# Optimization experiments

Hardware: AMD Instinct MI355X
Metric: run time of the kernel (lower is better)

## Reference

```python
import jax, jax.numpy as jnp
import numpy as np

N_NODES = 100000
N_EDGES = 1600000
NEG_SLOPE = 0.2
EPS = 1e-6


def setup_inputs() -> dict:
    key = jax.random.key(0)
    ks = jax.random.split(key, 14)
    s = 0.1  # weight init scale
    return {
        "x": jax.random.normal(ks[0], (N_NODES, 64), jnp.float32),
        "src": jax.random.randint(ks[1], (N_EDGES,), 0, N_NODES, jnp.int32),
        "dst": jax.random.randint(ks[2], (N_EDGES,), 0, N_NODES, jnp.int32),
        "W0": s * jax.random.normal(ks[3], (64, 128), jnp.float32),
        "al0": s * jax.random.normal(ks[4], (4, 32), jnp.float32),
        "ar0": s * jax.random.normal(ks[5], (4, 32), jnp.float32),
        "W1": s * jax.random.normal(ks[6], (128, 128), jnp.float32),
        "al1": s * jax.random.normal(ks[7], (4, 32), jnp.float32),
        "ar1": s * jax.random.normal(ks[8], (4, 32), jnp.float32),
        "resW1": s * jax.random.normal(ks[9], (128, 128), jnp.float32),
        "W2": s * jax.random.normal(ks[10], (128, 32), jnp.float32),
        "al2": s * jax.random.normal(ks[11], (1, 32), jnp.float32),
        "ar2": s * jax.random.normal(ks[12], (1, 32), jnp.float32),
        "resW2": s * jax.random.normal(ks[13], (128, 32), jnp.float32),
    }


def gat_conv(h, src, dst, W, al, ar, resW):
    """DGL-style GATConv. h: [N, Fin]; returns [N, H, D]."""
    H, D = al.shape
    feat = (h @ W).reshape(-1, H, D)                       # [N,H,D]
    el = jnp.sum(feat * al, axis=-1)                       # [N,H]
    er = jnp.sum(feat * ar, axis=-1)                       # [N,H]
    e = jax.nn.leaky_relu(el[src] + er[dst], NEG_SLOPE)    # [E,H]
    # segment softmax over destination nodes
    m = jax.ops.segment_max(e, dst, num_segments=N_NODES)  # [N,H]
    ex = jnp.exp(e - m[dst])                               # [E,H]
    denom = jax.ops.segment_sum(ex, dst, num_segments=N_NODES)
    alpha = ex / denom[dst]                                # [E,H]
    msg = alpha[:, :, None] * feat[src]                    # [E,H,D]
    rst = jax.ops.segment_sum(msg, dst, num_segments=N_NODES)  # [N,H,D]
    if resW is not None:
        rst = rst + (h @ resW).reshape(-1, H, D)
    return rst


def pairnorm_scs(x, scale=1.0):
    # 'PN-SCS' mode: scale-individually then center by original column mean
    col_mean = jnp.mean(x, axis=0)
    rownorm = jnp.sqrt(EPS + jnp.sum(x * x, axis=1, keepdims=True))
    return scale * x / rownorm - col_mean


def reference(x, src, dst, W0, al0, ar0, W1, al1, ar1, resW1, W2, al2, ar2, resW2):
    # layer 0: no residual, activation applied outside
    h = gat_conv(x, src, dst, W0, al0, ar0, None)          # [N,4,32]
    h = jax.nn.elu(h.reshape(h.shape[0], -1))              # [N,128]
    h = pairnorm_scs(h)
    # middle layer: residual + internal ELU (DGL applies activation inside),
    # then the outer loop flattens and applies ELU again
    h = jax.nn.elu(gat_conv(h, src, dst, W1, al1, ar1, resW1))  # [N,4,32]
    h = jax.nn.elu(h.reshape(h.shape[0], -1))              # [N,128]
    h = pairnorm_scs(h)
    # final layer: residual, mean over heads
    h = gat_conv(h, src, dst, W2, al2, ar2, resW2)         # [N,1,32]
    h = jnp.mean(h, axis=1)                                # [N,32]
    # dgl.mean_nodes readout on a single graph -> mean over nodes
    return jnp.mean(h, axis=0)                             # [32]
```

## Files before the change

kernel.cpp:

```cpp
#include <hip/hip_runtime.h>


typedef __attribute__((ext_vector_type(8))) short s8v;
typedef __attribute__((ext_vector_type(4))) float f4v;
typedef __attribute__((ext_vector_type(2))) float f2v;
typedef __attribute__((ext_vector_type(2))) _Float16 h2;
typedef __attribute__((ext_vector_type(4))) _Float16 h4;

__device__ __forceinline__ unsigned short f2bf(float f) {
  unsigned int x = __float_as_uint(f);
  x += 0x7fffu + ((x >> 16) & 1u);
  return (unsigned short)(x >> 16);
}
__device__ __forceinline__ float bf2f(unsigned short u) {
  return __uint_as_float(((unsigned int)u) << 16);
}
__device__ __forceinline__ unsigned short f2h(float f) {
  _Float16 h = (_Float16)f;
  return __builtin_bit_cast(unsigned short, h);
}
__device__ __forceinline__ unsigned char f2fp8(float v) {
  return (unsigned char)(__builtin_amdgcn_cvt_pk_fp8_f32(v, v, 0, false) & 0xff);
}
__device__ __forceinline__ float lrelu(float x) { return fmaxf(x, 0.2f * x); }
__device__ __forceinline__ float elu1(float x) { return x > 0.f ? x : expm1f(x); }

__global__ __launch_bounds__(256) void hist2_k(const int* __restrict__ dst, int* __restrict__ counts,
                                               int* __restrict__ bhist, int E, int NB, int chunk) {
  __shared__ int h[512];
  for (int b = threadIdx.x; b < NB; b += 256) h[b] = 0;
  __syncthreads();
  int e0 = blockIdx.x * chunk;
  int e1 = min(E, e0 + chunk);
  for (int e = e0 + threadIdx.x; e < e1; e += 256) {
    int d = dst[e];
    atomicAdd(&counts[d], 1);
    atomicAdd(&h[d >> 8], 1);
  }
  __syncthreads();
  for (int b = threadIdx.x; b < NB; b += 256)
    bhist[(size_t)b * gridDim.x + blockIdx.x] = h[b];
}

__global__ __launch_bounds__(256) void scanA(const int* __restrict__ counts, int* __restrict__ rsp,
                                             int* __restrict__ bsumA, int* __restrict__ bhist,
                                             int* __restrict__ bsumB, int NA, int NSEG, int nbA) {
  __shared__ int s[256];
  int t = threadIdx.x;
  bool isA = (int)blockIdx.x < nbA;
  int bb = isA ? (int)blockIdx.x : (int)blockIdx.x - nbA;
  const int* in = isA ? counts : bhist;
  int* out = isA ? rsp : bhist;
  int* bs = isA ? bsumA : bsumB;
  int Nn = isA ? NA : NSEG;
  int base = bb * 1024 + t * 4;
  int v0 = (base + 0 < Nn) ? in[base + 0] : 0;
  int v1 = (base + 1 < Nn) ? in[base + 1] : 0;
  int v2 = (base + 2 < Nn) ? in[base + 2] : 0;
  int v3 = (base + 3 < Nn) ? in[base + 3] : 0;
  if (isA) {
    v0 = (v0 + 15) & ~15;
    v1 = (v1 + 15) & ~15;
    v2 = (v2 + 15) & ~15;
    v3 = (v3 + 15) & ~15;
  }
  s[t] = v0 + v1 + v2 + v3;
  __syncthreads();
  for (int off = 1; off < 256; off <<= 1) {
    int xv = (t >= off) ? s[t - off] : 0;
    __syncthreads();
    s[t] += xv;
    __syncthreads();
  }
  int excl = t ? s[t - 1] : 0;
  if (t == 255) bs[bb] = s[255];
  if (base + 0 < Nn) { out[base + 0] = excl; excl += v0; }
  if (base + 1 < Nn) { out[base + 1] = excl; excl += v1; }
  if (base + 2 < Nn) { out[base + 2] = excl; excl += v2; }
  if (base + 3 < Nn) { out[base + 3] = excl; }
}

__global__ __launch_bounds__(256) void scanB(int* __restrict__ rsp, const int* __restrict__ bsumA,
                                             int* __restrict__ bhist, const int* __restrict__ bsumB,
                                             int NA, int NSEG, int nbA, int nbB) {
  __shared__ int s[256];
  int t = threadIdx.x;
  bool isA = (int)blockIdx.x < nbA;
  int bb = isA ? (int)blockIdx.x : (int)blockIdx.x - nbA;
  int* arr = isA ? rsp : bhist;
  const int* bs = isA ? bsumA : bsumB;
  int nb = isA ? nbA : nbB;
  int Nn = isA ? NA : NSEG;
  s[t] = (t < nb) ? bs[t] : 0;
  __syncthreads();
  for (int off = 1; off < 256; off <<= 1) {
    int xv = (t >= off) ? s[t - off] : 0;
    __syncthreads();
    s[t] += xv;
    __syncthreads();
  }
  int pref = bb ? s[bb - 1] : 0;
  if (pref != 0) {
    int base = bb * 1024 + t * 4;
    if (base + 0 < Nn) arr[base + 0] += pref;
    if (base + 1 < Nn) arr[base + 1] += pref;
    if (base + 2 < Nn) arr[base + 2] += pref;
    if (base + 3 < Nn) arr[base + 3] += pref;
  }
}

__global__ __launch_bounds__(256) void bscatter_k(const int* __restrict__ src, const int* __restrict__ dst,
                                                  const int* __restrict__ seg, int2* __restrict__ ebuf,
                                                  int E, int NB, int chunk) {
  __shared__ int cur[512];
  for (int b = threadIdx.x; b < NB; b += 256)
    cur[b] = seg[(size_t)b * gridDim.x + blockIdx.x];
  __syncthreads();
  int e0 = blockIdx.x * chunk;
  int e1 = min(E, e0 + chunk);
  for (int e = e0 + threadIdx.x; e < e1; e += 256) {
    int d = dst[e];
    int pos = atomicAdd(&cur[d >> 8], 1);
    int2 v; v.x = src[e]; v.y = d;
    ebuf[pos] = v;
  }
}

__global__ __launch_bounds__(256) void fscatter_k(const int2* __restrict__ ebuf, const int* __restrict__ seg,
                                                  const int* __restrict__ rsp, int* __restrict__ csr_src,
                                                  int E, int NB, int P2B, int Nn) {
  __shared__ int cur[256];
  int b = blockIdx.x;
  int node0 = b << 8;
  int node = node0 + threadIdx.x;
  if (node < Nn) cur[threadIdx.x] = rsp[node];
  __syncthreads();
  int bstart = seg[(size_t)b * P2B];
  int bend = (b + 1 < NB) ? seg[(size_t)(b + 1) * P2B] : E;
  for (int e = bstart + threadIdx.x; e < bend; e += 256) {
    int2 sd = ebuf[e];
    int pos = atomicAdd(&cur[sd.y - node0], 1);
    csr_src[pos] = sd.x;
  }
}

__device__ __forceinline__ void pack_one(const float* W, const float* al, const float* ar,
                                         const float* resW, unsigned short* out,
                                         int K, int M, int BF, int H, int RES0, int t) {
  int c = t / K, k = t - c * K;
  float v = 0.f;
  if (c < BF) {
    v = W[k * BF + c];
  } else if (c < BF + H) {
    int h = c - BF;
    float s = 0.f;
    for (int d = 0; d < 32; d++) s += W[k * BF + h * 32 + d] * al[h * 32 + d];
    v = s;
  } else if (c < BF + 2 * H) {
    int h = c - BF - H;
    float s = 0.f;
    for (int d = 0; d < 32; d++) s += W[k * BF + h * 32 + d] * ar[h * 32 + d];
    v = s;
  } else if (c >= RES0) {
    v = resW[k * (M - RES0) + (c - RES0)];
  }
  unsigned short hi = f2bf(v);
  out[c * K + k] = hi;
  out[M * K + c * K + k] = f2bf(v - bf2f(hi));
}

__global__ __launch_bounds__(256) void fill_all(const float* __restrict__ W0, const float* __restrict__ al0,
                                                const float* __restrict__ ar0,
                                                const float* __restrict__ W1, const float* __restrict__ al1,
                                                const float* __restrict__ ar1, const float* __restrict__ resW1,
                                                const float* __restrict__ W2, const float* __restrict__ al2,
                                                const float* __restrict__ ar2, const float* __restrict__ resW2,
                                                unsigned short* __restrict__ w0t, unsigned short* __restrict__ w1t,
                                                unsigned short* __restrict__ w2t) {
  const int n0 = 144 * 64, n1 = 272 * 128, n2 = 80 * 128;
  int t = blockIdx.x * 256 + threadIdx.x;
  if (t < n0) {
    pack_one(W0, al0, ar0, nullptr, w0t, 64, 144, 128, 4, 144, t);
  } else if (t < n0 + n1) {
    pack_one(W1, al1, ar1, resW1, w1t, 128, 272, 128, 4, 144, t - n0);
  } else if (t < n0 + n1 + n2) {
    pack_one(W2, al2, ar2, resW2, w2t, 128, 80, 32, 1, 48, t - n0 - n1);
  }
}

template <int K, int M, int R, int BF, int H, int RES0, bool AF32, bool CMW>
__global__ __launch_bounds__(256) void gemm_bf16(const void* __restrict__ Av,
                                                 const unsigned short* __restrict__ Bt,
                                                 const float* __restrict__ colsum, float invN,
                                                 unsigned char* __restrict__ feat8,
                                                 float* __restrict__ el, float* __restrict__ er,
                                                 unsigned short* __restrict__ resh, int nRowTiles) {
  __shared__ float cmw_s[M];
  if constexpr (CMW) {
    for (int cc = threadIdx.x; cc < M; cc += 256) {
      float s = 0.f;
      for (int k = 0; k < K; k++)
        s += colsum[k] * (bf2f(Bt[cc * K + k]) + bf2f(Bt[(size_t)M * K + cc * K + k]));
      cmw_s[cc] = s * invN;
    }
    __syncthreads();
  }
  int wv = (int)((blockIdx.x * blockDim.x + threadIdx.x) >> 6);
  int tile0 = wv * R;
  if (tile0 >= nRowTiles) return;
  int lane = threadIdx.x & 63;
  int r = lane & 15, q = lane >> 4;
  s8v afrag[R][K / 32];
#pragma unroll
  for (int rr = 0; rr < R; rr++) {
    if constexpr (AF32) {
      const float* arow = (const float*)Av + (size_t)((tile0 + rr) * 16 + r) * K + q * 8;
#pragma unroll
      for (int kk = 0; kk < K / 32; kk++) {
        s8v v;
#pragma unroll
        for (int j = 0; j < 8; j++) v[j] = (short)f2bf(arow[kk * 32 + j]);
        afrag[rr][kk] = v;
      }
    } else {
      const unsigned short* arow = (const unsigned short*)Av + (size_t)((tile0 + rr) * 16 + r) * K + q * 8;
#pragma unroll
      for (int kk = 0; kk < K / 32; kk++) afrag[rr][kk] = *(const s8v*)(arow + kk * 32);
    }
  }
#pragma unroll
  for (int ct = 0; ct < M / 16; ct++) {
    const unsigned short* brow = Bt + (size_t)(ct * 16 + r) * K + q * 8;
    s8v bhi[K / 32], blo[K / 32];
#pragma unroll
    for (int kk = 0; kk < K / 32; kk++) {
      bhi[kk] = *(const s8v*)(brow + kk * 32);
      blo[kk] = *(const s8v*)(brow + (size_t)M * K + kk * 32);
    }
    int col = ct * 16 + r;
    float cmwv = 0.f;
    if constexpr (CMW) cmwv = cmw_s[col];
#pragma unroll
    for (int rr = 0; rr < R; rr++) {
      f4v acc = {0.f, 0.f, 0.f, 0.f};
#pragma unroll
      for (int kk = 0; kk < K / 32; kk++) {
        acc = __builtin_amdgcn_mfma_f32_16x16x32_bf16(afrag[rr][kk], bhi[kk], acc, 0, 0, 0);
        acc = __builtin_amdgcn_mfma_f32_16x16x32_bf16(afrag[rr][kk], blo[kk], acc, 0, 0, 0);
      }
      int row0 = (tile0 + rr) * 16 + q * 4;
#pragma unroll
      for (int i = 0; i < 4; i++) {
        float v = acc[i] - cmwv;
        size_t row = (size_t)(row0 + i);
        if (col < BF) {
          feat8[row * BF + col] = f2fp8(v);
        } else if (col < BF + H) {
          el[row * H + (col - BF)] = v;
        } else if (col < BF + 2 * H) {
          er[row * H + (col - BF - H)] = v;
        } else if (RES0 < M && col >= RES0) {
          resh[row * (M - RES0) + (col - RES0)] = f2h(v);
        }
      }
    }
  }
}

template <int MODE>
__global__ __launch_bounds__(256) void aggregate4(const unsigned char* __restrict__ feat8,
                                                  const float* __restrict__ el4,
                                                  const float* __restrict__ er4,
                                                  const int* __restrict__ csr_src,
                                                  const int* __restrict__ rsp,
                                                  const int* __restrict__ counts,
                                                  const unsigned short* __restrict__ resh,
                                                  unsigned short* __restrict__ vbf,
                                                  float* __restrict__ rnrm, int Nn) {
  int n = (int)((blockIdx.x * blockDim.x + threadIdx.x) >> 6);
  if (n >= Nn) return;
  int lane = threadIdx.x & 63;
  int start = __builtin_amdgcn_readfirstlane(rsp[n]);
  int deg = __builtin_amdgcn_readfirstlane(counts[n]);
  int chunks = (deg + 15) >> 4;
  int slot = lane >> 2, h = lane & 3;
  float ern = er4[(size_t)n * 4 + h];
  int hl = lane >> 4;
  unsigned dby = (unsigned)lane << 1;
  f2v a01 = {0.f, 0.f};
  float dsum = 0.f;
  for (int c = 0; c < chunks; c++) {
    const int* csp = csr_src + start + (c << 4);
    int sA = csp[slot];
    float exv = 0.f;
    if (((c << 4) + slot) < deg) {
      float e = el4[(size_t)sA * 4 + h] + ern;
      exv = __expf(fmaxf(e, 0.2f * e));
    }
    dsum += exv;
    int sj[16];
#pragma unroll
    for (int j = 0; j < 16; j++) sj[j] = csp[j];
#pragma unroll
    for (int j = 0; j < 16; j++) {
      float aw = __shfl(exv, (j << 2) | hl);
      unsigned short u = *(const unsigned short*)(feat8 + (((unsigned)sj[j] << 7) + dby));
      f2v fv = __builtin_amdgcn_cvt_pk_f32_fp8((int)u, false);
      f2v aw2 = {aw, aw};
      a01 = __builtin_elementwise_fma(fv, aw2, a01);
    }
  }
#pragma unroll
  for (int off = 4; off < 64; off <<= 1) dsum += __shfl_xor(dsum, off);
  float inv = dsum > 0.f ? 1.f / dsum : 0.f;
  float invh = __shfl(inv, hl);
  float v0, v1;
  if (MODE == 1) {
    h2 rr = *(const h2*)(resh + (size_t)n * 128 + lane * 2);
    v0 = elu1(elu1(a01[0] * invh + (float)rr[0]));
    v1 = elu1(elu1(a01[1] * invh + (float)rr[1]));
  } else {
    v0 = elu1(a01[0] * invh);
    v1 = elu1(a01[1] * invh);
  }
  float ss = v0 * v0 + v1 * v1;
#pragma unroll
  for (int off = 1; off < 64; off <<= 1) ss += __shfl_xor(ss, off);
  float rn = sqrtf(1e-6f + ss);
  float ri = 1.f / rn;
  unsigned int pk = (unsigned int)f2bf(v0 * ri) | ((unsigned int)f2bf(v1 * ri) << 16);
  *(unsigned int*)((char*)vbf + ((size_t)n << 8) + (lane << 2)) = pk;
  if (lane == 0) rnrm[n] = rn;
}

__global__ __launch_bounds__(256) void aggregate1(const unsigned char* __restrict__ feat8,
                                                  const float* __restrict__ el1,
                                                  const float* __restrict__ er1,
                                                  const int* __restrict__ csr_src,
                                                  const int* __restrict__ rsp,
                                                  const int* __restrict__ counts,
                                                  const unsigned short* __restrict__ res2h,
                                                  float* __restrict__ out2, int Nn) {
  int n = (int)((blockIdx.x * blockDim.x + threadIdx.x) >> 6);
  if (n >= Nn) return;
  int lane = threadIdx.x & 63;
  int start = __builtin_amdgcn_readfirstlane(rsp[n]);
  int deg = __builtin_amdgcn_readfirstlane(counts[n]);
  int chunks = (deg + 15) >> 4;
  int l16 = lane & 15;
  float ern = er1[n];
  int g = lane >> 3;
  unsigned dofs4 = (unsigned)(lane & 7) << 2;
  f2v acc01 = {0.f, 0.f}, acc23 = {0.f, 0.f};
  float dsum = 0.f;
  for (int c = 0; c < chunks; c++) {
    const int* csp = csr_src + start + (c << 4);
    int sA = csp[l16];
    float exv = 0.f;
    if (((c << 4) + l16) < deg) exv = __expf(lrelu(el1[sA] + ern));
    dsum += exv;
#pragma unroll
    for (int t = 0; t < 2; t++) {
      int j = (t << 3) + g;
      int sj = __shfl(sA, j);
      float aw = __shfl(exv, j);
      f2v aw2 = {aw, aw};
      unsigned int u = *(const unsigned int*)(feat8 + (((unsigned)sj << 5) + dofs4));
      f2v fa = __builtin_amdgcn_cvt_pk_f32_fp8((int)u, false);
      f2v fb = __builtin_amdgcn_cvt_pk_f32_fp8((int)u, true);
      acc01 = __builtin_elementwise_fma(fa, aw2, acc01);
      acc23 = __builtin_elementwise_fma(fb, aw2, acc23);
    }
  }
#pragma unroll
  for (int off = 1; off < 16; off <<= 1) dsum += __shfl_xor(dsum, off);
  float inv = dsum > 0.f ? 1.f / dsum : 0.f;
#pragma unroll
  for (int off = 8; off < 64; off <<= 1) {
    acc01[0] += __shfl_xor(acc01[0], off);
    acc01[1] += __shfl_xor(acc01[1], off);
    acc23[0] += __shfl_xor(acc23[0], off);
    acc23[1] += __shfl_xor(acc23[1], off);
  }
  if (lane < 8) {
    h4 rr = *(const h4*)(res2h + (size_t)n * 32 + (lane << 2));
    float4 o;
    o.x = acc01[0] * inv + (float)rr[0];
    o.y = acc01[1] * inv + (float)rr[1];
    o.z = acc23[0] * inv + (float)rr[2];
    o.w = acc23[1] * inv + (float)rr[3];
    *(float4*)(out2 + (size_t)n * 32 + (lane << 2)) = o;
  }
}

__global__ __launch_bounds__(256) void colsum_k(const unsigned short* __restrict__ vbf,
                                                const float* __restrict__ rnrm,
                                                float* __restrict__ colsum, int Nn) {
  __shared__ float ls[256];
  int tid = threadIdx.x;
  int c = tid & 127, rsub = tid >> 7;
  float cs = 0.f;
  for (int r = blockIdx.x * 2 + rsub; r < Nn; r += gridDim.x * 2)
    cs += bf2f(vbf[(size_t)r * 128 + c]) * rnrm[r];
  ls[tid] = cs;
  __syncthreads();
  if (tid < 128) atomicAdd(&colsum[tid], ls[tid] + ls[tid + 128]);
}

__global__ __launch_bounds__(256) void final_reduce(const float* __restrict__ out2,
                                                    float* __restrict__ outsum, int Nn) {
  __shared__ float ls[32];
  if (threadIdx.x < 32) ls[threadIdx.x] = 0.f;
  __syncthreads();
  int d = threadIdx.x & 31, rl = threadIdx.x >> 5;
  float acc = 0.f;
  for (int n = blockIdx.x * 8 + rl; n < Nn; n += gridDim.x * 8)
    acc += out2[(size_t)n * 32 + d];
  atomicAdd(&ls[d], acc);
  __syncthreads();
  if (threadIdx.x < 32) atomicAdd(&outsum[threadIdx.x], ls[threadIdx.x]);
}

__global__ void finalize_k(const float* __restrict__ outsum, float* __restrict__ out, float invN) {
  int t = threadIdx.x;
  if (t < 32) out[t] = outsum[t] * invN;
}

extern "C" void kernel_launch(void* const* d_in, const int* in_sizes, int n_in,
                              void* d_out, int out_size, void* d_ws, size_t ws_size,
                              hipStream_t stream) {
  const float* x     = (const float*)d_in[0];
  const int*   src   = (const int*)d_in[1];
  const int*   dst   = (const int*)d_in[2];
  const float* W0    = (const float*)d_in[3];
  const float* al0   = (const float*)d_in[4];
  const float* ar0   = (const float*)d_in[5];
  const float* W1    = (const float*)d_in[6];
  const float* al1   = (const float*)d_in[7];
  const float* ar1   = (const float*)d_in[8];
  const float* resW1 = (const float*)d_in[9];
  const float* W2    = (const float*)d_in[10];
  const float* al2   = (const float*)d_in[11];
  const float* ar2   = (const float*)d_in[12];
  const float* resW2 = (const float*)d_in[13];
  const int N = in_sizes[0] / 64;
  const int E = in_sizes[1];
  const float invN = 1.f / (float)N;
  const int Emax = E + 15 * N + 1024;
  const int NB = (N + 255) >> 8;
  const int P2B = 512;
  const int chunk = (E + P2B - 1) / P2B;
  const int segN = NB * P2B;
  const int nbA = (N + 1023) / 1024;
  const int nbB = (segN + 1023) / 1024;

  char* p = (char*)d_ws;
  auto alloc = [&](size_t bytes) { char* r = p; p += (bytes + 255) & ~(size_t)255; return r; };

  char* zbase = p;
  int*   counts  = (int*)alloc((size_t)4 * N);
  float* colsumA = (float*)alloc(512);
  float* colsumB = (float*)alloc(512);
  float* outsum  = (float*)alloc(128);
  size_t zbytes = (size_t)(p - zbase);

  int* rsp   = (int*)alloc((size_t)4 * N);
  int* bsumA = (int*)alloc(1024);
  int* bhist = (int*)alloc((size_t)4 * segN);
  int* bsumB = (int*)alloc(1024);
  int2* ebuf = (int2*)alloc((size_t)8 * E);
  int* csr_src = (int*)alloc((size_t)4 * Emax);
  unsigned char*  feat8 = (unsigned char*)alloc((size_t)N * 128);
  unsigned short* vbf   = (unsigned short*)alloc((size_t)2 * N * 128);
  unsigned short* resh  = (unsigned short*)alloc((size_t)2 * N * 128);
  unsigned short* w0t = (unsigned short*)alloc((size_t)2 * 2 * 144 * 64);
  unsigned short* w1t = (unsigned short*)alloc((size_t)2 * 2 * 272 * 128);
  unsigned short* w2t = (unsigned short*)alloc((size_t)2 * 2 * 80 * 128);
  float* el4  = (float*)alloc((size_t)16 * N);
  float* er4  = (float*)alloc((size_t)16 * N);
  float* rnrm = (float*)alloc((size_t)4 * N);
  float* out2 = (float*)alloc((size_t)4 * N * 32);

  hipMemsetAsync(zbase, 0, zbytes, stream);
  hipMemsetAsync(csr_src, 0, (size_t)4 * Emax, stream);

  hist2_k<<<P2B, 256, 0, stream>>>(dst, counts, bhist, E, NB, chunk);
  scanA<<<nbA + nbB, 256, 0, stream>>>(counts, rsp, bsumA, bhist, bsumB, N, segN, nbA);
  scanB<<<nbA + nbB, 256, 0, stream>>>(rsp, bsumA, bhist, bsumB, N, segN, nbA, nbB);
  bscatter_k<<<P2B, 256, 0, stream>>>(src, dst, bhist, ebuf, E, NB, chunk);
  fscatter_k<<<NB, 256, 0, stream>>>(ebuf, bhist, rsp, csr_src, E, NB, P2B, N);

  const int packTot = 144 * 64 + 272 * 128 + 80 * 128;
  fill_all<<<(packTot + 255) / 256, 256, 0, stream>>>(W0, al0, ar0, W1, al1, ar1, resW1,
                                                      W2, al2, ar2, resW2, w0t, w1t, w2t);

  const int rowTiles = N / 16;
  const int gblocks = (rowTiles / 5 + 3) / 4;
  const int aggblocks = (N + 3) / 4;

  gemm_bf16<64, 144, 5, 128, 4, 144, true, false><<<gblocks, 256, 0, stream>>>(
      x, w0t, nullptr, invN, feat8, el4, er4, nullptr, rowTiles);
  aggregate4<0><<<aggblocks, 256, 0, stream>>>(feat8, el4, er4, csr_src, rsp, counts, nullptr, vbf, rnrm, N);
  colsum_k<<<512, 256, 0, stream>>>(vbf, rnrm, colsumA, N);

  gemm_bf16<128, 272, 5, 128, 4, 144, false, true><<<gblocks, 256, 0, stream>>>(
      vbf, w1t, colsumA, invN, feat8, el4, er4, resh, rowTiles);
  aggregate4<1><<<aggblocks, 256, 0, stream>>>(feat8, el4, er4, csr_src, rsp, counts, resh, vbf, rnrm, N);
  colsum_k<<<512, 256, 0, stream>>>(vbf, rnrm, colsumB, N);

  gemm_bf16<128, 80, 5, 32, 1, 48, false, true><<<gblocks, 256, 0, stream>>>(
      vbf, w2t, colsumB, invN, feat8, el4, er4, resh, rowTiles);
  aggregate1<<<aggblocks, 256, 0, stream>>>(feat8, el4, er4, csr_src, rsp, counts, resh, out2, N);
  final_reduce<<<512, 256, 0, stream>>>(out2, outsum, N);
  finalize_k<<<1, 64, 0, stream>>>(outsum, (float*)d_out, invN);
}
```

Before: 565.5 us.

## Fuse weight packing into histogram, pack edge buffer, prefetch el in aggregation

Merges the weight-packing kernel into the degree-histogram launch as extra blocks, which removes one kernel launch. It shrinks the bucketed edge buffer from int2 to a single 32-bit word holding src<<8 plus the low byte of dst, halving scatter traffic. It also software-prefetches the next chunk's el value in the aggregation loops to hide gather latency, and swaps expm1f for __expf-1 in ELU. The packed encoding assumes node ids fit in 24 bits, and the ELU change loses some precision for small negative inputs.

```diff
diff --git a/kernel.cpp b/kernel.cpp
--- a/kernel.cpp
+++ b/kernel.cpp
@@ -23,23 +23,68 @@
   return (unsigned char)(__builtin_amdgcn_cvt_pk_fp8_f32(v, v, 0, false) & 0xff);
 }
 __device__ __forceinline__ float lrelu(float x) { return fmaxf(x, 0.2f * x); }
-__device__ __forceinline__ float elu1(float x) { return x > 0.f ? x : expm1f(x); }
-
-__global__ __launch_bounds__(256) void hist2_k(const int* __restrict__ dst, int* __restrict__ counts,
-                                               int* __restrict__ bhist, int E, int NB, int chunk) {
-  __shared__ int h[512];
-  for (int b = threadIdx.x; b < NB; b += 256) h[b] = 0;
-  __syncthreads();
-  int e0 = blockIdx.x * chunk;
-  int e1 = min(E, e0 + chunk);
-  for (int e = e0 + threadIdx.x; e < e1; e += 256) {
-    int d = dst[e];
-    atomicAdd(&counts[d], 1);
-    atomicAdd(&h[d >> 8], 1);
-  }
-  __syncthreads();
-  for (int b = threadIdx.x; b < NB; b += 256)
-    bhist[(size_t)b * gridDim.x + blockIdx.x] = h[b];
+__device__ __forceinline__ float elu1(float x) { return x > 0.f ? x : __expf(x) - 1.f; }
+
+__device__ __forceinline__ void pack_one(const float* W, const float* al, const float* ar,
+                                         const float* resW, unsigned short* out,
+                                         int K, int M, int BF, int H, int RES0, int t) {
+  int c = t / K, k = t - c * K;
+  float v = 0.f;
+  if (c < BF) {
+    v = W[k * BF + c];
+  } else if (c < BF + H) {
+    int h = c - BF;
+    float s = 0.f;
+    for (int d = 0; d < 32; d++) s += W[k * BF + h * 32 + d] * al[h * 32 + d];
+    v = s;
+  } else if (c < BF + 2 * H) {
+    int h = c - BF - H;
+    float s = 0.f;
+    for (int d = 0; d < 32; d++) s += W[k * BF + h * 32 + d] * ar[h * 32 + d];
+    v = s;
+  } else if (c >= RES0) {
+    v = resW[k * (M - RES0) + (c - RES0)];
+  }
+  unsigned short hi = f2bf(v);
+  out[c * K + k] = hi;
+  out[M * K + c * K + k] = f2bf(v - bf2f(hi));
+}
+
+__global__ __launch_bounds__(256) void hist_pack_k(const int* __restrict__ dst, int* __restrict__ counts,
+                                                   int* __restrict__ bhist, int E, int NB, int chunk, int P2B,
+                                                   const float* __restrict__ W0, const float* __restrict__ al0,
+                                                   const float* __restrict__ ar0,
+                                                   const float* __restrict__ W1, const float* __restrict__ al1,
+                                                   const float* __restrict__ ar1, const float* __restrict__ resW1,
+                                                   const float* __restrict__ W2, const float* __restrict__ al2,
+                                                   const float* __restrict__ ar2, const float* __restrict__ resW2,
+                                                   unsigned short* __restrict__ w0t, unsigned short* __restrict__ w1t,
+                                                   unsigned short* __restrict__ w2t) {
+  if ((int)blockIdx.x < P2B) {
+    __shared__ int h[512];
+    for (int b = threadIdx.x; b < NB; b += 256) h[b] = 0;
+    __syncthreads();
+    int e0 = blockIdx.x * chunk;
+    int e1 = min(E, e0 + chunk);
+    for (int e = e0 + threadIdx.x; e < e1; e += 256) {
+      int d = dst[e];
+      atomicAdd(&counts[d], 1);
+      atomicAdd(&h[d >> 8], 1);
+    }
+    __syncthreads();
+    for (int b = threadIdx.x; b < NB; b += 256)
+      bhist[(size_t)b * P2B + blockIdx.x] = h[b];
+  } else {
+    const int n0 = 144 * 64, n1 = 272 * 128, n2 = 80 * 128;
+    int t = ((int)blockIdx.x - P2B) * 256 + threadIdx.x;
+    if (t < n0) {
+      pack_one(W0, al0, ar0, nullptr, w0t, 64, 144, 128, 4, 144, t);
+    } else if (t < n0 + n1) {
+      pack_one(W1, al1, ar1, resW1, w1t, 128, 272, 128, 4, 144, t - n0);
+    } else if (t < n0 + n1 + n2) {
+      pack_one(W2, al2, ar2, resW2, w2t, 128, 80, 32, 1, 48, t - n0 - n1);
+    }
+  }
 }
 
 __global__ __launch_bounds__(256) void scanA(const int* __restrict__ counts, int* __restrict__ rsp,
@@ -110,7 +155,7 @@
 }
 
 __global__ __launch_bounds__(256) void bscatter_k(const int* __restrict__ src, const int* __restrict__ dst,
-                                                  const int* __restrict__ seg, int2* __restrict__ ebuf,
+                                                  const int* __restrict__ seg, unsigned int* __restrict__ ebuf,
                                                   int E, int NB, int chunk) {
   __shared__ int cur[512];
   for (int b = threadIdx.x; b < NB; b += 256)
@@ -121,12 +166,12 @@
   for (int e = e0 + threadIdx.x; e < e1; e += 256) {
     int d = dst[e];
     int pos = atomicAdd(&cur[d >> 8], 1);
-    int2 v; v.x = src[e]; v.y = d;
-    ebuf[pos] = v;
-  }
-}
-
-__global__ __launch_bounds__(256) void fscatter_k(const int2* __restrict__ ebuf, const int* __restrict__ seg,
+    ebuf[pos] = ((unsigned int)src[e] << 8) | (unsigned int)(d & 255);
+  }
+}
+
+__global__ __launch_bounds__(256) void fscatter_k(const unsigned int* __restrict__ ebuf,
+                                                  const int* __restrict__ seg,
                                                   const int* __restrict__ rsp, int* __restrict__ csr_src,
                                                   int E, int NB, int P2B, int Nn) {
   __shared__ int cur[256];
@@ -138,53 +183,9 @@
   int bstart = seg[(size_t)b * P2B];
   int bend = (b + 1 < NB) ? seg[(size_t)(b + 1) * P2B] : E;
   for (int e = bstart + threadIdx.x; e < bend; e += 256) {
-    int2 sd = ebuf[e];
-    int pos = atomicAdd(&cur[sd.y - node0], 1);
-    csr_src[pos] = sd.x;
-  }
-}
-
-__device__ __forceinline__ void pack_one(const float* W, const float* al, const float* ar,
-                                         const float* resW, unsigned short* out,
-                                         int K, int M, int BF, int H, int RES0, int t) {
-  int c = t / K, k = t - c * K;
-  float v = 0.f;
-  if (c < BF) {
-    v = W[k * BF + c];
-  } else if (c < BF + H) {
-    int h = c - BF;
-    float s = 0.f;
-    for (int d = 0; d < 32; d++) s += W[k * BF + h * 32 + d] * al[h * 32 + d];
-    v = s;
-  } else if (c < BF + 2 * H) {
-    int h = c - BF - H;
-    float s = 0.f;
-    for (int d = 0; d < 32; d++) s += W[k * BF + h * 32 + d] * ar[h * 32 + d];
-    v = s;
-  } else if (c >= RES0) {
-    v = resW[k * (M - RES0) + (c - RES0)];
-  }
-  unsigned short hi = f2bf(v);
-  out[c * K + k] = hi;
-  out[M * K + c * K + k] = f2bf(v - bf2f(hi));
-}
-
-__global__ __launch_bounds__(256) void fill_all(const float* __restrict__ W0, const float* __restrict__ al0,
-                                                const float* __restrict__ ar0,
-                                                const float* __restrict__ W1, const float* __restrict__ al1,
-                                                const float* __restrict__ ar1, const float* __restrict__ resW1,
-                                                const float* __restrict__ W2, const float* __restrict__ al2,
-                                                const float* __restrict__ ar2, const float* __restrict__ resW2,
-                                                unsigned short* __restrict__ w0t, unsigned short* __restrict__ w1t,
-                                                unsigned short* __restrict__ w2t) {
-  const int n0 = 144 * 64, n1 = 272 * 128, n2 = 80 * 128;
-  int t = blockIdx.x * 256 + threadIdx.x;
-  if (t < n0) {
-    pack_one(W0, al0, ar0, nullptr, w0t, 64, 144, 128, 4, 144, t);
-  } else if (t < n0 + n1) {
-    pack_one(W1, al1, ar1, resW1, w1t, 128, 272, 128, 4, 144, t - n0);
-  } else if (t < n0 + n1 + n2) {
-    pack_one(W2, al2, ar2, resW2, w2t, 128, 80, 32, 1, 48, t - n0 - n1);
+    unsigned int sd = ebuf[e];
+    int pos = atomicAdd(&cur[sd & 255u], 1);
+    csr_src[pos] = (int)(sd >> 8);
   }
 }
 
@@ -289,18 +290,16 @@
   unsigned dby = (unsigned)lane << 1;
   f2v a01 = {0.f, 0.f};
   float dsum = 0.f;
+  float elv = el4[(size_t)csr_src[start + slot] * 4 + h];
   for (int c = 0; c < chunks; c++) {
     const int* csp = csr_src + start + (c << 4);
-    int sA = csp[slot];
-    float exv = 0.f;
-    if (((c << 4) + slot) < deg) {
-      float e = el4[(size_t)sA * 4 + h] + ern;
-      exv = __expf(fmaxf(e, 0.2f * e));
-    }
+    int sj[16];
+#pragma unroll
+    for (int j = 0; j < 16; j++) sj[j] = csp[j];
+    float e = elv + ern;
+    float exv = (((c << 4) + slot) < deg) ? __expf(fmaxf(e, 0.2f * e)) : 0.f;
     dsum += exv;
-    int sj[16];
-#pragma unroll
-    for (int j = 0; j < 16; j++) sj[j] = csp[j];
+    if (c + 1 < chunks) elv = el4[(size_t)csp[16 + slot] * 4 + h];
 #pragma unroll
     for (int j = 0; j < 16; j++) {
       float aw = __shfl(exv, (j << 2) | hl);
@@ -353,16 +352,21 @@
   unsigned dofs4 = (unsigned)(lane & 7) << 2;
   f2v acc01 = {0.f, 0.f}, acc23 = {0.f, 0.f};
   float dsum = 0.f;
+  int sA = csr_src[start + l16];
+  float elv = el1[sA];
   for (int c = 0; c < chunks; c++) {
     const int* csp = csr_src + start + (c << 4);
-    int sA = csp[l16];
-    float exv = 0.f;
-    if (((c << 4) + l16) < deg) exv = __expf(lrelu(el1[sA] + ern));
+    float exv = (((c << 4) + l16) < deg) ? __expf(lrelu(elv + ern)) : 0.f;
     dsum += exv;
+    int sAc = sA;
+    if (c + 1 < chunks) {
+      sA = csp[16 + l16];
+      elv = el1[sA];
+    }
 #pragma unroll
     for (int t = 0; t < 2; t++) {
       int j = (t << 3) + g;
-      int sj = __shfl(sA, j);
+      int sj = __shfl(sAc, j);
       float aw = __shfl(exv, j);
       f2v aw2 = {aw, aw};
       unsigned int u = *(const unsigned int*)(feat8 + (((unsigned)sj << 5) + dofs4));
@@ -468,7 +472,7 @@
   int* bsumA = (int*)alloc(1024);
   int* bhist = (int*)alloc((size_t)4 * segN);
   int* bsumB = (int*)alloc(1024);
-  int2* ebuf = (int2*)alloc((size_t)8 * E);
+  unsigned int* ebuf = (unsigned int*)alloc((size_t)4 * E);
   int* csr_src = (int*)alloc((size_t)4 * Emax);
   unsigned char*  feat8 = (unsigned char*)alloc((size_t)N * 128);
   unsigned short* vbf   = (unsigned short*)alloc((size_t)2 * N * 128);
@@ -484,15 +488,15 @@
   hipMemsetAsync(zbase, 0, zbytes, stream);
   hipMemsetAsync(csr_src, 0, (size_t)4 * Emax, stream);
 
-  hist2_k<<<P2B, 256, 0, stream>>>(dst, counts, bhist, E, NB, chunk);
+  const int packTot = 144 * 64 + 272 * 128 + 80 * 128;
+  const int packBlocks = (packTot + 255) / 256;
+  hist_pack_k<<<P2B + packBlocks, 256, 0, stream>>>(dst, counts, bhist, E, NB, chunk, P2B,
+                                                    W0, al0, ar0, W1, al1, ar1, resW1,
+                                                    W2, al2, ar2, resW2, w0t, w1t, w2t);
   scanA<<<nbA + nbB, 256, 0, stream>>>(counts, rsp, bsumA, bhist, bsumB, N, segN, nbA);
   scanB<<<nbA + nbB, 256, 0, stream>>>(rsp, bsumA, bhist, bsumB, N, segN, nbA, nbB);
   bscatter_k<<<P2B, 256, 0, stream>>>(src, dst, bhist, ebuf, E, NB, chunk);
   fscatter_k<<<NB, 256, 0, stream>>>(ebuf, bhist, rsp, csr_src, E, NB, P2B, N);
-
-  const int packTot = 144 * 64 + 272 * 128 + 80 * 128;
-  fill_all<<<(packTot + 255) / 256, 256, 0, stream>>>(W0, al0, ar0, W1, al1, ar1, resW1,
-                                                      W2, al2, ar2, resW2, w0t, w1t, w2t);
 
   const int rowTiles = N / 16;
   const int gblocks = (rowTiles / 5 + 3) / 4;
```

Result: faster. 546.1 us (-3.4%).
